# Optimization experiments

Hardware: AMD Instinct MI355X
Metric: run time of the kernel (lower is better)

The kernel has to match this reference:

```python
import jax, jax.numpy as jnp
import numpy as np
import math

B_SZ, T_LEN = 2, 1024
D_MODEL, D_STATE, D_CONV, EXPAND = 1024, 16, 4, 2
D_INNER = EXPAND * D_MODEL            # 2048
DT_RANK = math.ceil(D_MODEL / 16)     # 64


def setup_inputs() -> dict:
    key = jax.random.key(0)
    ks = jax.random.split(key, 10)
    f32 = jnp.float32
    x = jax.random.normal(ks[0], (B_SZ, T_LEN, D_MODEL), f32)
    norm_w = jnp.ones((D_MODEL,), f32)
    in_proj_w = jax.random.normal(ks[1], (2 * D_INNER, D_MODEL), f32) / np.sqrt(D_MODEL)
    conv_w = jax.random.uniform(ks[2], (D_INNER, 1, D_CONV), f32, -0.5, 0.5)
    conv_b = jax.random.uniform(ks[3], (D_INNER,), f32, -0.5, 0.5)
    x_proj_w = jax.random.normal(ks[4], (DT_RANK + 2 * D_STATE, D_INNER), f32) / np.sqrt(D_INNER)
    dt_std = DT_RANK ** (-0.5)
    dt_proj_w = jax.random.uniform(ks[5], (D_INNER, DT_RANK), f32, -dt_std, dt_std)
    # dt bias init: softplus(bias) lands in [dt_min, dt_max]
    dt = jnp.exp(jax.random.uniform(ks[6], (D_INNER,), f32) * (np.log(0.1) - np.log(0.001)) + np.log(0.001))
    dt_proj_b = dt + jnp.log(-jnp.expm1(-dt))
    A_log = jnp.log(jnp.tile(jnp.arange(1, D_STATE + 1, dtype=f32)[None, :], (D_INNER, 1)))
    D_param = jnp.ones((D_INNER,), f32)
    out_proj_w = jax.random.normal(ks[7], (D_MODEL, D_INNER), f32) / np.sqrt(D_INNER)
    return {"x": x, "norm_w": norm_w, "in_proj_w": in_proj_w, "conv_w": conv_w,
            "conv_b": conv_b, "x_proj_w": x_proj_w, "dt_proj_w": dt_proj_w,
            "dt_proj_b": dt_proj_b, "A_log": A_log, "D_param": D_param,
            "out_proj_w": out_proj_w}


def _mamba_forward(x, norm_w, in_proj_w, conv_w, conv_b, x_proj_w,
                   dt_proj_w, dt_proj_b, A_log, D_param, out_proj_w):
    residual = x
    # RMSNorm (torch nn.RMSNorm, eps=None -> finfo eps)
    eps = jnp.finfo(x.dtype).eps
    xn = x * jax.lax.rsqrt(jnp.mean(x * x, axis=-1, keepdims=True) + eps) * norm_w
    # input projection -> ssm stream + gate
    xz = xn @ in_proj_w.T                     # [B,T,2*d_inner]
    x_s, z = xz[..., :D_INNER], xz[..., D_INNER:]
    # causal depthwise conv1d (pad left d_conv-1, matches padding=d_conv-1 then [:T])
    u = jax.lax.conv_general_dilated(
        x_s.transpose(0, 2, 1), conv_w, window_strides=(1,),
        padding=[(D_CONV - 1, 0)], dimension_numbers=("NCH", "OIH", "NCH"),
        feature_group_count=D_INNER) + conv_b[None, :, None]
    u = jax.nn.silu(u).transpose(0, 2, 1)     # [B,T,d_inner]
    # input-dependent SSM params
    x_dbc = u @ x_proj_w.T
    dt_raw = x_dbc[..., :DT_RANK]
    B_ssm = x_dbc[..., DT_RANK:DT_RANK + D_STATE]
    C_ssm = x_dbc[..., DT_RANK + D_STATE:]
    delta = jax.nn.softplus(dt_raw @ dt_proj_w.T + dt_proj_b)   # [B,T,d_inner]
    A = -jnp.exp(A_log)                                         # [d_inner,d_state]
    # discretize
    dA = jnp.exp(jnp.einsum("bti,is->btis", delta, A))          # [B,T,i,s]
    dBu = jnp.einsum("bti,bts->btis", delta * u, B_ssm)         # [B,T,i,s]
    # sequential scan over time (lax.scan, carry h [B,i,s])
    def step(h, inp):
        dA_t, dBu_t, C_t = inp
        h = dA_t * h + dBu_t
        y_t = jnp.einsum("bis,bs->bi", h, C_t)
        return h, y_t
    h0 = jnp.zeros((x.shape[0], D_INNER, D_STATE), x.dtype)
    _, ys = jax.lax.scan(step, h0,
                         (dA.transpose(1, 0, 2, 3), dBu.transpose(1, 0, 2, 3),
                          C_ssm.transpose(1, 0, 2)))
    y = ys.transpose(1, 0, 2) + u * D_param                     # [B,T,d_inner]
    y = y * jax.nn.silu(z)
    return y @ out_proj_w.T + residual


def reference(x, norm_w, in_proj_w, conv_w, conv_b, x_proj_w,
              dt_proj_w, dt_proj_b, A_log, D_param, out_proj_w):
    return _mamba_forward(x, norm_w, in_proj_w, conv_w, conv_b, x_proj_w,
                          dt_proj_w, dt_proj_b, A_log, D_param, out_proj_w)
```

## Files before the change

### kernel.cpp

```cpp
#include <hip/hip_runtime.h>
#include <math.h>

#define B_SZ 2
#define T_LEN 1024
#define D_MODEL 1024
#define D_STATE 16
#define D_INNER 2048
#define DT_RANK 64
#define NTOK (B_SZ * T_LEN)
#define XPROJ_OUT 96
#define XPROJ_LD 128
#define NCHUNK 32
#define CHUNK_L (T_LEN / NCHUNK)
#define NSPLIT 32

typedef __attribute__((ext_vector_type(8))) short bf16x8;
typedef __attribute__((ext_vector_type(4))) float f32x4;

__device__ __forceinline__ float sigmoidf_(float x) { return 1.f / (1.f + __expf(-x)); }

__device__ __forceinline__ unsigned f2bf_u(float f) {
    unsigned u = __float_as_uint(f);
    return (u + 0x7FFFu + ((u >> 16) & 1u)) >> 16;
}
__device__ __forceinline__ float bf2f(unsigned short u) {
    return __uint_as_float((unsigned)u << 16);
}

__device__ __forceinline__ void gload_lds16(const void* g, void* l) {
    __builtin_amdgcn_global_load_lds((const __attribute__((address_space(1))) unsigned*)g,
                                     (__attribute__((address_space(3))) unsigned*)l,
                                     16, 0, 0);
}

__global__ __launch_bounds__(256) void k_prep(const float* __restrict__ x,
                                              const float* __restrict__ norm_w,
                                              const float* __restrict__ w_in,
                                              const float* __restrict__ w_out,
                                              const float* __restrict__ w_x,
                                              const float* __restrict__ w_dt,
                                              unsigned short* __restrict__ xn,
                                              unsigned* __restrict__ wib,
                                              unsigned* __restrict__ wob,
                                              unsigned* __restrict__ wxb,
                                              unsigned* __restrict__ wdtb) {
    __shared__ float red[4];
    int blk = blockIdx.x;
    if (blk < 2048) {
        const float* xr = x + (size_t)blk * D_MODEL;
        int i = threadIdx.x * 4;
        float4 xv = *(const float4*)(xr + i);
        float s = xv.x * xv.x + xv.y * xv.y + xv.z * xv.z + xv.w * xv.w;
#pragma unroll
        for (int m = 1; m <= 32; m <<= 1) s += __shfl_xor(s, m);
        if ((threadIdx.x & 63) == 0) red[threadIdx.x >> 6] = s;
        __syncthreads();
        float tot = red[0] + red[1] + red[2] + red[3];
        float scale = rsqrtf(tot * (1.f / D_MODEL) + 1.1920929e-07f);
        float4 wv = *(const float4*)(norm_w + i);
        uint2 o;
        o.x = f2bf_u(xv.x * scale * wv.x) | (f2bf_u(xv.y * scale * wv.y) << 16);
        o.y = f2bf_u(xv.z * scale * wv.z) | (f2bf_u(xv.w * scale * wv.w) << 16);
        *(uint2*)(xn + (size_t)blk * D_MODEL + i) = o;
        return;
    }
    blk -= 2048;
    const float* src;
    unsigned* dst;
    int lidx;
    if (blk < 2048) {
        src = w_in; dst = wib; lidx = blk * 256 + threadIdx.x;
    } else if (blk < 3072) {
        src = w_out; dst = wob; lidx = (blk - 2048) * 256 + threadIdx.x;
    } else if (blk < 3200) {
        dst = wxb; lidx = (blk - 3072) * 256 + threadIdx.x;
        if (lidx * 8 >= 96 * 2048) {
            uint4 z = {0, 0, 0, 0};
            ((uint4*)dst)[lidx] = z;
            return;
        }
        src = w_x;
    } else {
        src = w_dt; dst = wdtb; lidx = (blk - 3200) * 256 + threadIdx.x;
    }
    float4 a = ((const float4*)src)[lidx * 2];
    float4 b = ((const float4*)src)[lidx * 2 + 1];
    uint4 o;
    o.x = f2bf_u(a.x) | (f2bf_u(a.y) << 16);
    o.y = f2bf_u(a.z) | (f2bf_u(a.w) << 16);
    o.z = f2bf_u(b.x) | (f2bf_u(b.y) << 16);
    o.w = f2bf_u(b.z) | (f2bf_u(b.w) << 16);
    ((uint4*)dst)[lidx] = o;
}


template <int BN, int CW, int EPI>
__global__ __launch_bounds__(256) void gemm_bf16(const unsigned short* __restrict__ A,
                                                 const unsigned short* __restrict__ B,
                                                 void* __restrict__ Cv, int ldc, int K,
                                                 const float* __restrict__ res) {
    constexpr int RW = 4 / CW;
    constexpr int MI = (128 / RW) / 16;
    constexpr int NJ = (BN / CW) / 16;
    __shared__ __align__(16) unsigned short As[128 * 64];
    __shared__ __align__(16) unsigned short Bs[BN * 64];
    int tid = threadIdx.x;
    int lane = tid & 63, wv = tid >> 6;
    int wr = wv / CW, wc = wv % CW;
    int lm = lane & 15, q = lane >> 4;
    int sw = lm & 7;
    int m0 = blockIdx.x * 128, n0 = blockIdx.y * BN;
    f32x4 acc[MI][NJ] = {};
    for (int k0 = 0; k0 < K; k0 += 64) {
#pragma unroll
        for (int it = 0; it < 4; ++it) {
            int chunk = it * 256 + tid;
            int cc = (chunk & 7) ^ ((chunk >> 3) & 7);
            const unsigned short* g = A + (size_t)(m0 + (chunk >> 3)) * K + k0 + cc * 8;
            char* l = (char*)As + (it * 256 + wv * 64) * 16 + lane * 16;
            gload_lds16(g, l);
        }
#pragma unroll
        for (int it = 0; it < BN / 32; ++it) {
            int chunk = it * 256 + tid;
            int cc = (chunk & 7) ^ ((chunk >> 3) & 7);
            const unsigned short* g = B + (size_t)(n0 + (chunk >> 3)) * K + k0 + cc * 8;
            char* l = (char*)Bs + (it * 256 + wv * 64) * 16 + lane * 16;
            gload_lds16(g, l);
        }
        __syncthreads();
#pragma unroll
        for (int h = 0; h < 2; ++h) {
            bf16x8 af[MI], bfr[NJ];
#pragma unroll
            for (int i = 0; i < MI; ++i)
                af[i] = *(const bf16x8*)(As + (wr * MI * 16 + i * 16 + lm) * 64 +
                                         (((h << 2) + q) ^ sw) * 8);
#pragma unroll
            for (int j = 0; j < NJ; ++j)
                bfr[j] = *(const bf16x8*)(Bs + (wc * NJ * 16 + j * 16 + lm) * 64 +
                                          (((h << 2) + q) ^ sw) * 8);
#pragma unroll
            for (int i = 0; i < MI; ++i)
#pragma unroll
                for (int j = 0; j < NJ; ++j)
                    acc[i][j] = __builtin_amdgcn_mfma_f32_16x16x32_bf16(af[i], bfr[j], acc[i][j], 0, 0, 0);
        }
        __syncthreads();
    }
#pragma unroll
    for (int i = 0; i < MI; ++i) {
#pragma unroll
        for (int j = 0; j < NJ; ++j) {
#pragma unroll
            for (int r = 0; r < 4; ++r) {
                int row = m0 + wr * MI * 16 + i * 16 + q * 4 + r;
                int col = n0 + wc * NJ * 16 + j * 16 + lm;
                float v = acc[i][j][r];
                if (EPI == 1) {
                    v += res[col];
                    v = (v > 20.f) ? v : log1pf(__expf(v));
                    ((unsigned short*)Cv)[(size_t)row * ldc + col] = (unsigned short)f2bf_u(v);
                } else {
                    if (n0 >= D_INNER) v = v * sigmoidf_(v);
                    ((unsigned short*)Cv)[(size_t)row * ldc + col] = (unsigned short)f2bf_u(v);
                }
            }
        }
    }
}

__global__ __launch_bounds__(256) void gemm_sq64(const unsigned short* __restrict__ A,
                                                 const unsigned short* __restrict__ B,
                                                 float* __restrict__ C, int ldc, int K,
                                                 const float* __restrict__ res) {
    __shared__ __align__(16) unsigned short As[64 * 64];
    __shared__ __align__(16) unsigned short Bs[64 * 64];
    int tid = threadIdx.x;
    int lane = tid & 63, wv = tid >> 6;
    int wr = wv >> 1, wc = wv & 1;
    int lm = lane & 15, q = lane >> 4;
    int sw = lm & 7;
    int m0 = blockIdx.x * 64, n0 = blockIdx.y * 64;
    f32x4 acc[2][2] = {};
    for (int k0 = 0; k0 < K; k0 += 64) {
#pragma unroll
        for (int it = 0; it < 2; ++it) {
            int chunk = it * 256 + tid;
            int cc = (chunk & 7) ^ ((chunk >> 3) & 7);
            const unsigned short* g = A + (size_t)(m0 + (chunk >> 3)) * K + k0 + cc * 8;
            char* l = (char*)As + (it * 256 + wv * 64) * 16 + lane * 16;
            gload_lds16(g, l);
        }
#pragma unroll
        for (int it = 0; it < 2; ++it) {
            int chunk = it * 256 + tid;
            int cc = (chunk & 7) ^ ((chunk >> 3) & 7);
            const unsigned short* g = B + (size_t)(n0 + (chunk >> 3)) * K + k0 + cc * 8;
            char* l = (char*)Bs + (it * 256 + wv * 64) * 16 + lane * 16;
            gload_lds16(g, l);
        }
        __syncthreads();
#pragma unroll
        for (int h = 0; h < 2; ++h) {
            bf16x8 af[2], bfr[2];
#pragma unroll
            for (int i = 0; i < 2; ++i)
                af[i] = *(const bf16x8*)(As + (wr * 32 + i * 16 + lm) * 64 +
                                         (((h << 2) + q) ^ sw) * 8);
#pragma unroll
            for (int j = 0; j < 2; ++j)
                bfr[j] = *(const bf16x8*)(Bs + (wc * 32 + j * 16 + lm) * 64 +
                                          (((h << 2) + q) ^ sw) * 8);
#pragma unroll
            for (int i = 0; i < 2; ++i)
#pragma unroll
                for (int j = 0; j < 2; ++j)
                    acc[i][j] = __builtin_amdgcn_mfma_f32_16x16x32_bf16(af[i], bfr[j], acc[i][j], 0, 0, 0);
        }
        __syncthreads();
    }
#pragma unroll
    for (int i = 0; i < 2; ++i)
#pragma unroll
        for (int j = 0; j < 2; ++j)
#pragma unroll
            for (int r = 0; r < 4; ++r) {
                int row = m0 + wr * 32 + i * 16 + q * 4 + r;
                int col = n0 + wc * 32 + j * 16 + lm;
                C[(size_t)row * ldc + col] = acc[i][j][r] + res[(size_t)row * ldc + col];
            }
}

__global__ __launch_bounds__(256) void xproj_gemm(const unsigned short* __restrict__ A,
                                                  const unsigned short* __restrict__ B,
                                                  unsigned short* __restrict__ part) {
    constexpr int MI = 4, NJ = 4;
    __shared__ __align__(16) unsigned short As[128 * 64];
    __shared__ __align__(16) unsigned short Bs[128 * 64];
    int tid = threadIdx.x;
    int lane = tid & 63, wv = tid >> 6;
    int wr = wv >> 1, wc = wv & 1;
    int lm = lane & 15, q = lane >> 4;
    int sw = lm & 7;
    int m0 = blockIdx.x * 128;
    int k0 = blockIdx.y * 64;
    f32x4 acc[MI][NJ] = {};
#pragma unroll
    for (int it = 0; it < 4; ++it) {
        int chunk = it * 256 + tid;
        int cc = (chunk & 7) ^ ((chunk >> 3) & 7);
        const unsigned short* g = A + (size_t)(m0 + (chunk >> 3)) * D_INNER + k0 + cc * 8;
        char* l = (char*)As + (it * 256 + wv * 64) * 16 + lane * 16;
        gload_lds16(g, l);
    }
#pragma unroll
    for (int it = 0; it < 4; ++it) {
        int chunk = it * 256 + tid;
        int cc = (chunk & 7) ^ ((chunk >> 3) & 7);
        const unsigned short* g = B + (size_t)(chunk >> 3) * D_INNER + k0 + cc * 8;
        char* l = (char*)Bs + (it * 256 + wv * 64) * 16 + lane * 16;
        gload_lds16(g, l);
    }
    __syncthreads();
#pragma unroll
    for (int h = 0; h < 2; ++h) {
        bf16x8 af[MI], bfr[NJ];
#pragma unroll
        for (int i = 0; i < MI; ++i)
            af[i] = *(const bf16x8*)(As + (wr * 64 + i * 16 + lm) * 64 + (((h << 2) + q) ^ sw) * 8);
#pragma unroll
        for (int j = 0; j < NJ; ++j)
            bfr[j] = *(const bf16x8*)(Bs + (wc * 64 + j * 16 + lm) * 64 + (((h << 2) + q) ^ sw) * 8);
#pragma unroll
        for (int i = 0; i < MI; ++i)
#pragma unroll
            for (int j = 0; j < NJ; ++j)
                acc[i][j] = __builtin_amdgcn_mfma_f32_16x16x32_bf16(af[i], bfr[j], acc[i][j], 0, 0, 0);
    }
    unsigned short* dst = part + (size_t)blockIdx.y * (NTOK * XPROJ_LD);
#pragma unroll
    for (int i = 0; i < MI; ++i)
#pragma unroll
        for (int j = 0; j < NJ; ++j)
#pragma unroll
            for (int r = 0; r < 4; ++r) {
                int row = m0 + wr * 64 + i * 16 + q * 4 + r;
                int col = wc * 64 + j * 16 + lm;
                dst[(size_t)row * XPROJ_LD + col] = (unsigned short)f2bf_u(acc[i][j][r]);
            }
}

__global__ __launch_bounds__(256) void k_xred(const unsigned short* __restrict__ part,
                                              float* __restrict__ dbc,
                                              unsigned short* __restrict__ dtrawb) {
    int idx4 = blockIdx.x * 256 + threadIdx.x;
    float s0 = 0.f, s1 = 0.f, s2 = 0.f, s3 = 0.f;
#pragma unroll
    for (int sp = 0; sp < NSPLIT; ++sp) {
        uint2 v = *(const uint2*)(part + (size_t)sp * (NTOK * XPROJ_LD) + idx4 * 4);
        s0 += __uint_as_float(v.x << 16);
        s1 += __uint_as_float(v.x & 0xFFFF0000u);
        s2 += __uint_as_float(v.y << 16);
        s3 += __uint_as_float(v.y & 0xFFFF0000u);
    }
    float4 sv = {s0, s1, s2, s3};
    *(float4*)(dbc + idx4 * 4) = sv;
    int col = (idx4 * 4) & (XPROJ_LD - 1);
    if (col < DT_RANK) {
        int row = (idx4 * 4) >> 7;
        uint2 o;
        o.x = f2bf_u(s0) | (f2bf_u(s1) << 16);
        o.y = f2bf_u(s2) | (f2bf_u(s3) << 16);
        *(uint2*)(dtrawb + (size_t)row * DT_RANK + col) = o;
    }
}

__global__ __launch_bounds__(256) void k_conv(const unsigned short* __restrict__ xz,
                                              const float* __restrict__ cw,
                                              const float* __restrict__ cb,
                                              unsigned short* __restrict__ ub) {
    int idx = blockIdx.x * 256 + threadIdx.x;
    int c = idx & (D_INNER - 1);
    int t = (idx >> 11) & (T_LEN - 1);
    int b = idx >> 21;
    const unsigned short* xs = xz + (size_t)b * T_LEN * 2 * D_INNER + c;
    float4 wv = *(const float4*)(cw + c * 4);
    float s = cb[c];
    if (t >= 3) s = fmaf(bf2f(xs[(size_t)(t - 3) * 2 * D_INNER]), wv.x, s);
    if (t >= 2) s = fmaf(bf2f(xs[(size_t)(t - 2) * 2 * D_INNER]), wv.y, s);
    if (t >= 1) s = fmaf(bf2f(xs[(size_t)(t - 1) * 2 * D_INNER]), wv.z, s);
    s = fmaf(bf2f(xs[(size_t)t * 2 * D_INNER]), wv.w, s);
    float v = s * sigmoidf_(s);
    ub[idx] = (unsigned short)f2bf_u(v);
}

__global__ __launch_bounds__(256) void k_scan1(const unsigned short* __restrict__ delta,
                                               const unsigned short* __restrict__ ub,
                                               const float* __restrict__ dbc,
                                               const float* __restrict__ A_log,
                                               float* __restrict__ Pbuf,
                                               float* __restrict__ Hbuf) {
    int tid = threadIdx.x;
    int c = blockIdx.x * 256 + tid;
    int b = blockIdx.y >> 5, chunk = blockIdx.y & 31;
    int t0 = chunk * CHUNK_L;
    __shared__ float bc[CHUNK_L][32];
    {
        int t = tid >> 3, col = (tid & 7) * 4;
        const float* src = dbc + ((size_t)b * T_LEN + t0 + t) * XPROJ_LD + DT_RANK + col;
        *(float4*)&bc[t][col] = *(const float4*)src;
    }
    __syncthreads();
    float A[16];
#pragma unroll
    for (int s4 = 0; s4 < 4; ++s4) {
        float4 av = *(const float4*)(A_log + (size_t)c * D_STATE + s4 * 4);
        A[s4 * 4 + 0] = -__expf(av.x);
        A[s4 * 4 + 1] = -__expf(av.y);
        A[s4 * 4 + 2] = -__expf(av.z);
        A[s4 * 4 + 3] = -__expf(av.w);
    }
    const unsigned short* dp = delta + ((size_t)b * T_LEN + t0) * D_INNER + c;
    const unsigned short* up = ub + ((size_t)b * T_LEN + t0) * D_INNER + c;
    float h[16] = {};
    float sumd = 0.f;
#pragma unroll 4
    for (int t = 0; t < CHUNK_L; ++t) {
        float dv = bf2f(dp[(size_t)t * D_INNER]);
        float uv = bf2f(up[(size_t)t * D_INNER]);
        float du = dv * uv;
        sumd += dv;
#pragma unroll
        for (int s = 0; s < 16; ++s) {
            float da = __expf(dv * A[s]);
            h[s] = fmaf(da, h[s], du * bc[t][s]);
        }
    }
    size_t o = ((size_t)((b * NCHUNK + chunk) * D_INNER) + c) * 16;
#pragma unroll
    for (int s4 = 0; s4 < 4; ++s4) {
        float4 hv = {h[s4 * 4], h[s4 * 4 + 1], h[s4 * 4 + 2], h[s4 * 4 + 3]};
        *(float4*)(Hbuf + o + s4 * 4) = hv;
        float4 pv = {__expf(A[s4 * 4] * sumd), __expf(A[s4 * 4 + 1] * sumd),
                     __expf(A[s4 * 4 + 2] * sumd), __expf(A[s4 * 4 + 3] * sumd)};
        *(float4*)(Pbuf + o + s4 * 4) = pv;
    }
}

__global__ __launch_bounds__(256) void k_scan2(const float* __restrict__ Pbuf,
                                               const float* __restrict__ Hbuf,
                                               float* __restrict__ Sbuf) {
    int idx = blockIdx.x * 256 + threadIdx.x;
    int b = idx >> 15, r = idx & 32767;
    size_t base = (size_t)b * NCHUNK * (D_INNER * 16) + r;
    float p[NCHUNK], hl[NCHUNK];
#pragma unroll
    for (int ch = 0; ch < NCHUNK; ++ch) {
        size_t o = base + (size_t)ch * (D_INNER * 16);
        p[ch] = Pbuf[o];
        hl[ch] = Hbuf[o];
    }
    float h = 0.f;
#pragma unroll
    for (int ch = 0; ch < NCHUNK; ++ch) {
        Sbuf[base + (size_t)ch * (D_INNER * 16)] = h;
        h = fmaf(p[ch], h, hl[ch]);
    }
}

__global__ __launch_bounds__(256) void k_scan3(const unsigned short* __restrict__ delta,
                                               const unsigned short* __restrict__ ub,
                                               const float* __restrict__ dbc,
                                               const unsigned short* __restrict__ xz,
                                               const float* __restrict__ A_log,
                                               const float* __restrict__ Dp,
                                               const float* __restrict__ Sbuf,
                                               unsigned short* __restrict__ yb) {
    int tid = threadIdx.x;
    int c = blockIdx.x * 256 + tid;
    int b = blockIdx.y >> 5, chunk = blockIdx.y & 31;
    int t0 = chunk * CHUNK_L;
    __shared__ float bc[CHUNK_L][32];
    {
        int t = tid >> 3, col = (tid & 7) * 4;
        const float* src = dbc + ((size_t)b * T_LEN + t0 + t) * XPROJ_LD + DT_RANK + col;
        *(float4*)&bc[t][col] = *(const float4*)src;
    }
    __syncthreads();
    float A[16];
#pragma unroll
    for (int s4 = 0; s4 < 4; ++s4) {
        float4 av = *(const float4*)(A_log + (size_t)c * D_STATE + s4 * 4);
        A[s4 * 4 + 0] = -__expf(av.x);
        A[s4 * 4 + 1] = -__expf(av.y);
        A[s4 * 4 + 2] = -__expf(av.z);
        A[s4 * 4 + 3] = -__expf(av.w);
    }
    float Dc = Dp[c];
    float h[16];
    size_t ho = ((size_t)((b * NCHUNK + chunk) * D_INNER) + c) * 16;
#pragma unroll
    for (int s4 = 0; s4 < 4; ++s4) {
        float4 hv = *(const float4*)(Sbuf + ho + s4 * 4);
        h[s4 * 4] = hv.x; h[s4 * 4 + 1] = hv.y; h[s4 * 4 + 2] = hv.z; h[s4 * 4 + 3] = hv.w;
    }
    const unsigned short* dp = delta + ((size_t)b * T_LEN + t0) * D_INNER + c;
    const unsigned short* up = ub + ((size_t)b * T_LEN + t0) * D_INNER + c;
    const unsigned short* zp = xz + ((size_t)b * T_LEN + t0) * 2 * D_INNER + D_INNER + c;
    unsigned short* yp = yb + ((size_t)b * T_LEN + t0) * D_INNER + c;
#pragma unroll 2
    for (int t = 0; t < CHUNK_L; ++t) {
        float dv = bf2f(dp[(size_t)t * D_INNER]);
        float uv = bf2f(up[(size_t)t * D_INNER]);
        float sz = bf2f(zp[(size_t)t * 2 * D_INNER]);
        float du = dv * uv;
        float y = Dc * uv;
#pragma unroll
        for (int s = 0; s < 16; ++s) {
            float da = __expf(dv * A[s]);
            h[s] = fmaf(da, h[s], du * bc[t][s]);
            y = fmaf(h[s], bc[t][16 + s], y);
        }
        yp[(size_t)t * D_INNER] = (unsigned short)f2bf_u(y * sz);
    }
}

extern "C" void kernel_launch(void* const* d_in, const int* in_sizes, int n_in,
                              void* d_out, int out_size, void* d_ws, size_t ws_size,
                              hipStream_t stream) {
    const float* x         = (const float*)d_in[0];
    const float* norm_w    = (const float*)d_in[1];
    const float* in_proj_w = (const float*)d_in[2];
    const float* conv_w    = (const float*)d_in[3];
    const float* conv_b    = (const float*)d_in[4];
    const float* x_proj_w  = (const float*)d_in[5];
    const float* dt_proj_w = (const float*)d_in[6];
    const float* dt_proj_b = (const float*)d_in[7];
    const float* A_log     = (const float*)d_in[8];
    const float* D_param   = (const float*)d_in[9];
    const float* out_proj_w= (const float*)d_in[10];
    float* out = (float*)d_out;

    float* ws = (float*)d_ws;
    unsigned short* xzb    = (unsigned short*)(ws);
    unsigned short* ub     = (unsigned short*)(ws + 4194304);
    unsigned short* yb     = (unsigned short*)(ws + 6291456);
    unsigned short* partb  = (unsigned short*)(ws + 8388608);
    float*          dbc    = ws + 12582912;
    unsigned short* deltab = (unsigned short*)(ws + 12845056);
    float*          Pbuf   = ws + 14942208;
    float*          Hbuf   = ws + 17039360;
    float*          Sbuf   = ws + 19136512;
    unsigned short* wib    = (unsigned short*)(ws + 21233664);
    unsigned short* wob    = (unsigned short*)(ws + 23330816);
    unsigned short* wxb    = (unsigned short*)(ws + 24379392);
    unsigned short* wdtb   = (unsigned short*)(ws + 24510464);
    unsigned short* dtrawb = (unsigned short*)(ws + 24576000);
    unsigned short* xnb    = (unsigned short*)(ws + 24641536);

    k_prep<<<5312, 256, 0, stream>>>(x, norm_w, in_proj_w, out_proj_w, x_proj_w, dt_proj_w,
                                     xnb, (unsigned*)wib, (unsigned*)wob, (unsigned*)wxb,
                                     (unsigned*)wdtb);
    gemm_bf16<128, 2, 3><<<dim3(NTOK / 128, 4096 / 128), 256, 0, stream>>>(
        xnb, wib, xzb, 2 * D_INNER, D_MODEL, nullptr);
    k_conv<<<(NTOK * D_INNER) / 256, 256, 0, stream>>>(xzb, conv_w, conv_b, ub);
    xproj_gemm<<<dim3(NTOK / 128, NSPLIT), 256, 0, stream>>>(ub, wxb, partb);
    k_xred<<<(NTOK * XPROJ_LD) / 1024, 256, 0, stream>>>(partb, dbc, dtrawb);
    gemm_bf16<64, 1, 1><<<dim3(NTOK / 128, D_INNER / 64), 256, 0, stream>>>(
        dtrawb, wdtb, deltab, D_INNER, DT_RANK, dt_proj_b);
    k_scan1<<<dim3(D_INNER / 256, B_SZ * NCHUNK), 256, 0, stream>>>(deltab, ub, dbc, A_log,
                                                                    Pbuf, Hbuf);
    k_scan2<<<(B_SZ * D_INNER * D_STATE) / 256, 256, 0, stream>>>(Pbuf, Hbuf, Sbuf);
    k_scan3<<<dim3(D_INNER / 256, B_SZ * NCHUNK), 256, 0, stream>>>(deltab, ub, dbc, xzb, A_log,
                                                                    D_param, Sbuf, yb);
    gemm_sq64<<<dim3(NTOK / 64, D_MODEL / 64), 256, 0, stream>>>(
        yb, wob, out, D_MODEL, D_INNER, x);

    (void)in_sizes; (void)n_in; (void)out_size; (void)ws_size;
}
```

Measured before the change: 250.7 us.

## Halve x_proj split-K, vectorize conv, route out_proj through templated GEMM

The x_proj GEMM now loops over two 64-wide K slices per block, which halves the split-K factor and shrinks the partial buffer the reduction must read. The conv kernel handles four channels per thread with vector loads and stores, cutting the thread count and the number of memory instructions. The dedicated 64x64 out_proj GEMM is replaced by the generic gemm_bf16 template with a new fp32 residual epilogue, using 128-row tiles. These are several independent changes to different kernels, and the larger out_proj tiles reduce the number of blocks in flight.

```diff
diff --git a/kernel.cpp b/kernel.cpp
--- a/kernel.cpp
+++ b/kernel.cpp
@@ -12,7 +12,7 @@
 #define XPROJ_LD 128
 #define NCHUNK 32
 #define CHUNK_L (T_LEN / NCHUNK)
-#define NSPLIT 32
+#define NSPLIT 16
 
 typedef __attribute__((ext_vector_type(8))) short bf16x8;
 typedef __attribute__((ext_vector_type(4))) float f32x4;
@@ -157,7 +157,9 @@
                 int row = m0 + wr * MI * 16 + i * 16 + q * 4 + r;
                 int col = n0 + wc * NJ * 16 + j * 16 + lm;
                 float v = acc[i][j][r];
-                if (EPI == 1) {
+                if (EPI == 0) {
+                    ((float*)Cv)[(size_t)row * ldc + col] = v + res[(size_t)row * ldc + col];
+                } else if (EPI == 1) {
                     v += res[col];
                     v = (v > 20.f) ? v : log1pf(__expf(v));
                     ((unsigned short*)Cv)[(size_t)row * ldc + col] = (unsigned short)f2bf_u(v);
@@ -168,68 +170,6 @@
             }
         }
     }
-}
-
-__global__ __launch_bounds__(256) void gemm_sq64(const unsigned short* __restrict__ A,
-                                                 const unsigned short* __restrict__ B,
-                                                 float* __restrict__ C, int ldc, int K,
-                                                 const float* __restrict__ res) {
-    __shared__ __align__(16) unsigned short As[64 * 64];
-    __shared__ __align__(16) unsigned short Bs[64 * 64];
-    int tid = threadIdx.x;
-    int lane = tid & 63, wv = tid >> 6;
-    int wr = wv >> 1, wc = wv & 1;
-    int lm = lane & 15, q = lane >> 4;
-    int sw = lm & 7;
-    int m0 = blockIdx.x * 64, n0 = blockIdx.y * 64;
-    f32x4 acc[2][2] = {};
-    for (int k0 = 0; k0 < K; k0 += 64) {
-#pragma unroll
-        for (int it = 0; it < 2; ++it) {
-            int chunk = it * 256 + tid;
-            int cc = (chunk & 7) ^ ((chunk >> 3) & 7);
-            const unsigned short* g = A + (size_t)(m0 + (chunk >> 3)) * K + k0 + cc * 8;
-            char* l = (char*)As + (it * 256 + wv * 64) * 16 + lane * 16;
-            gload_lds16(g, l);
-        }
-#pragma unroll
-        for (int it = 0; it < 2; ++it) {
-            int chunk = it * 256 + tid;
-            int cc = (chunk & 7) ^ ((chunk >> 3) & 7);
-            const unsigned short* g = B + (size_t)(n0 + (chunk >> 3)) * K + k0 + cc * 8;
-            char* l = (char*)Bs + (it * 256 + wv * 64) * 16 + lane * 16;
-            gload_lds16(g, l);
-        }
-        __syncthreads();
-#pragma unroll
-        for (int h = 0; h < 2; ++h) {
-            bf16x8 af[2], bfr[2];
-#pragma unroll
-            for (int i = 0; i < 2; ++i)
-                af[i] = *(const bf16x8*)(As + (wr * 32 + i * 16 + lm) * 64 +
-                                         (((h << 2) + q) ^ sw) * 8);
-#pragma unroll
-            for (int j = 0; j < 2; ++j)
-                bfr[j] = *(const bf16x8*)(Bs + (wc * 32 + j * 16 + lm) * 64 +
-                                          (((h << 2) + q) ^ sw) * 8);
-#pragma unroll
-            for (int i = 0; i < 2; ++i)
-#pragma unroll
-                for (int j = 0; j < 2; ++j)
-                    acc[i][j] = __builtin_amdgcn_mfma_f32_16x16x32_bf16(af[i], bfr[j], acc[i][j], 0, 0, 0);
-        }
-        __syncthreads();
-    }
-#pragma unroll
-    for (int i = 0; i < 2; ++i)
-#pragma unroll
-        for (int j = 0; j < 2; ++j)
-#pragma unroll
-            for (int r = 0; r < 4; ++r) {
-                int row = m0 + wr * 32 + i * 16 + q * 4 + r;
-                int col = n0 + wc * 32 + j * 16 + lm;
-                C[(size_t)row * ldc + col] = acc[i][j][r] + res[(size_t)row * ldc + col];
-            }
 }
 
 __global__ __launch_bounds__(256) void xproj_gemm(const unsigned short* __restrict__ A,
@@ -244,39 +184,42 @@
     int lm = lane & 15, q = lane >> 4;
     int sw = lm & 7;
     int m0 = blockIdx.x * 128;
-    int k0 = blockIdx.y * 64;
     f32x4 acc[MI][NJ] = {};
-#pragma unroll
-    for (int it = 0; it < 4; ++it) {
-        int chunk = it * 256 + tid;
-        int cc = (chunk & 7) ^ ((chunk >> 3) & 7);
-        const unsigned short* g = A + (size_t)(m0 + (chunk >> 3)) * D_INNER + k0 + cc * 8;
-        char* l = (char*)As + (it * 256 + wv * 64) * 16 + lane * 16;
-        gload_lds16(g, l);
-    }
-#pragma unroll
-    for (int it = 0; it < 4; ++it) {
-        int chunk = it * 256 + tid;
-        int cc = (chunk & 7) ^ ((chunk >> 3) & 7);
-        const unsigned short* g = B + (size_t)(chunk >> 3) * D_INNER + k0 + cc * 8;
-        char* l = (char*)Bs + (it * 256 + wv * 64) * 16 + lane * 16;
-        gload_lds16(g, l);
-    }
-    __syncthreads();
-#pragma unroll
-    for (int h = 0; h < 2; ++h) {
-        bf16x8 af[MI], bfr[NJ];
-#pragma unroll
-        for (int i = 0; i < MI; ++i)
-            af[i] = *(const bf16x8*)(As + (wr * 64 + i * 16 + lm) * 64 + (((h << 2) + q) ^ sw) * 8);
-#pragma unroll
-        for (int j = 0; j < NJ; ++j)
-            bfr[j] = *(const bf16x8*)(Bs + (wc * 64 + j * 16 + lm) * 64 + (((h << 2) + q) ^ sw) * 8);
-#pragma unroll
-        for (int i = 0; i < MI; ++i)
+    for (int ks = 0; ks < 2; ++ks) {
+        int k0 = blockIdx.y * 128 + ks * 64;
+#pragma unroll
+        for (int it = 0; it < 4; ++it) {
+            int chunk = it * 256 + tid;
+            int cc = (chunk & 7) ^ ((chunk >> 3) & 7);
+            const unsigned short* g = A + (size_t)(m0 + (chunk >> 3)) * D_INNER + k0 + cc * 8;
+            char* l = (char*)As + (it * 256 + wv * 64) * 16 + lane * 16;
+            gload_lds16(g, l);
+        }
+#pragma unroll
+        for (int it = 0; it < 4; ++it) {
+            int chunk = it * 256 + tid;
+            int cc = (chunk & 7) ^ ((chunk >> 3) & 7);
+            const unsigned short* g = B + (size_t)(chunk >> 3) * D_INNER + k0 + cc * 8;
+            char* l = (char*)Bs + (it * 256 + wv * 64) * 16 + lane * 16;
+            gload_lds16(g, l);
+        }
+        __syncthreads();
+#pragma unroll
+        for (int h = 0; h < 2; ++h) {
+            bf16x8 af[MI], bfr[NJ];
+#pragma unroll
+            for (int i = 0; i < MI; ++i)
+                af[i] = *(const bf16x8*)(As + (wr * 64 + i * 16 + lm) * 64 + (((h << 2) + q) ^ sw) * 8);
 #pragma unroll
             for (int j = 0; j < NJ; ++j)
-                acc[i][j] = __builtin_amdgcn_mfma_f32_16x16x32_bf16(af[i], bfr[j], acc[i][j], 0, 0, 0);
+                bfr[j] = *(const bf16x8*)(Bs + (wc * 64 + j * 16 + lm) * 64 + (((h << 2) + q) ^ sw) * 8);
+#pragma unroll
+            for (int i = 0; i < MI; ++i)
+#pragma unroll
+                for (int j = 0; j < NJ; ++j)
+                    acc[i][j] = __builtin_amdgcn_mfma_f32_16x16x32_bf16(af[i], bfr[j], acc[i][j], 0, 0, 0);
+        }
+        __syncthreads();
     }
     unsigned short* dst = part + (size_t)blockIdx.y * (NTOK * XPROJ_LD);
 #pragma unroll
@@ -321,18 +264,37 @@
                                               const float* __restrict__ cb,
                                               unsigned short* __restrict__ ub) {
     int idx = blockIdx.x * 256 + threadIdx.x;
-    int c = idx & (D_INNER - 1);
-    int t = (idx >> 11) & (T_LEN - 1);
-    int b = idx >> 21;
-    const unsigned short* xs = xz + (size_t)b * T_LEN * 2 * D_INNER + c;
-    float4 wv = *(const float4*)(cw + c * 4);
-    float s = cb[c];
-    if (t >= 3) s = fmaf(bf2f(xs[(size_t)(t - 3) * 2 * D_INNER]), wv.x, s);
-    if (t >= 2) s = fmaf(bf2f(xs[(size_t)(t - 2) * 2 * D_INNER]), wv.y, s);
-    if (t >= 1) s = fmaf(bf2f(xs[(size_t)(t - 1) * 2 * D_INNER]), wv.z, s);
-    s = fmaf(bf2f(xs[(size_t)t * 2 * D_INNER]), wv.w, s);
-    float v = s * sigmoidf_(s);
-    ub[idx] = (unsigned short)f2bf_u(v);
+    int c4 = (idx & (D_INNER / 4 - 1)) * 4;
+    int t = (idx >> 9) & (T_LEN - 1);
+    int b = idx >> 19;
+    const unsigned short* xs = xz + (size_t)b * T_LEN * 2 * D_INNER + c4;
+    float4 w[4];
+#pragma unroll
+    for (int i = 0; i < 4; ++i) w[i] = ((const float4*)cw)[c4 + i];
+    float4 cbv = *(const float4*)(cb + c4);
+    float s[4] = {cbv.x, cbv.y, cbv.z, cbv.w};
+#pragma unroll
+    for (int k = 0; k < 4; ++k) {
+        int tt = t - 3 + k;
+        if (tt >= 0) {
+            ushort4 xv = *(const ushort4*)(xs + (size_t)tt * 2 * D_INNER);
+            float fx0 = bf2f(xv.x), fx1 = bf2f(xv.y), fx2 = bf2f(xv.z), fx3 = bf2f(xv.w);
+            float w0 = (k == 0) ? w[0].x : (k == 1) ? w[0].y : (k == 2) ? w[0].z : w[0].w;
+            float w1 = (k == 0) ? w[1].x : (k == 1) ? w[1].y : (k == 2) ? w[1].z : w[1].w;
+            float w2 = (k == 0) ? w[2].x : (k == 1) ? w[2].y : (k == 2) ? w[2].z : w[2].w;
+            float w3 = (k == 0) ? w[3].x : (k == 1) ? w[3].y : (k == 2) ? w[3].z : w[3].w;
+            s[0] = fmaf(fx0, w0, s[0]);
+            s[1] = fmaf(fx1, w1, s[1]);
+            s[2] = fmaf(fx2, w2, s[2]);
+            s[3] = fmaf(fx3, w3, s[3]);
+        }
+    }
+    ushort4 o;
+    o.x = (unsigned short)f2bf_u(s[0] * sigmoidf_(s[0]));
+    o.y = (unsigned short)f2bf_u(s[1] * sigmoidf_(s[1]));
+    o.z = (unsigned short)f2bf_u(s[2] * sigmoidf_(s[2]));
+    o.w = (unsigned short)f2bf_u(s[3] * sigmoidf_(s[3]));
+    *(ushort4*)(ub + (size_t)(b * T_LEN + t) * D_INNER + c4) = o;
 }
 
 __global__ __launch_bounds__(256) void k_scan1(const unsigned short* __restrict__ delta,
@@ -504,7 +466,7 @@
                                      (unsigned*)wdtb);
     gemm_bf16<128, 2, 3><<<dim3(NTOK / 128, 4096 / 128), 256, 0, stream>>>(
         xnb, wib, xzb, 2 * D_INNER, D_MODEL, nullptr);
-    k_conv<<<(NTOK * D_INNER) / 256, 256, 0, stream>>>(xzb, conv_w, conv_b, ub);
+    k_conv<<<(NTOK * D_INNER / 4) / 256, 256, 0, stream>>>(xzb, conv_w, conv_b, ub);
     xproj_gemm<<<dim3(NTOK / 128, NSPLIT), 256, 0, stream>>>(ub, wxb, partb);
     k_xred<<<(NTOK * XPROJ_LD) / 1024, 256, 0, stream>>>(partb, dbc, dtrawb);
     gemm_bf16<64, 1, 1><<<dim3(NTOK / 128, D_INNER / 64), 256, 0, stream>>>(
@@ -514,8 +476,8 @@
     k_scan2<<<(B_SZ * D_INNER * D_STATE) / 256, 256, 0, stream>>>(Pbuf, Hbuf, Sbuf);
     k_scan3<<<dim3(D_INNER / 256, B_SZ * NCHUNK), 256, 0, stream>>>(deltab, ub, dbc, xzb, A_log,
                                                                     D_param, Sbuf, yb);
-    gemm_sq64<<<dim3(NTOK / 64, D_MODEL / 64), 256, 0, stream>>>(
-        yb, wob, out, D_MODEL, D_INNER, x);
+    gemm_bf16<64, 2, 0><<<dim3(NTOK / 128, D_MODEL / 64), 256, 0, stream>>>(
+        yb, wob, (void*)out, D_MODEL, D_INNER, x);
 
     (void)in_sizes; (void)n_in; (void)out_size; (void)ws_size;
 }
```

New measurement: 256.6 us. 2.4% more time.
